# Optimization experiments

Measured on AMD Instinct MI355X. Metric: run time of the kernel, lower is better.

## Reference

```python
import jax, jax.numpy as jnp
import numpy as np

N = 50000
E = 600000
IN_CH = 128
HID = 64


def setup_inputs() -> dict:
    key = jax.random.key(0)
    ks = jax.random.split(key, 8)
    x = jax.random.normal(ks[0], (N, IN_CH), dtype=jnp.float32)
    edge_index = jax.random.randint(ks[1], (2, E), 0, N, dtype=jnp.int64)
    s = 1.0 / np.sqrt(IN_CH)
    W_rel = jax.random.uniform(ks[2], (IN_CH, HID), jnp.float32, -s, s)
    b_rel = jax.random.uniform(ks[3], (HID,), jnp.float32, -s, s)
    W_root = jax.random.uniform(ks[4], (IN_CH, HID), jnp.float32, -s, s)
    sh = 1.0 / np.sqrt(HID)
    W_dec = jax.random.uniform(ks[5], (HID, IN_CH), jnp.float32, -sh, sh)
    b_dec = jax.random.uniform(ks[6], (IN_CH,), jnp.float32, -sh, sh)
    return {"x": x, "edge_index": edge_index, "W_rel": W_rel, "b_rel": b_rel,
            "W_root": W_root, "W_dec": W_dec, "b_dec": b_dec}


def reference(x, edge_index, W_rel, b_rel, W_root, W_dec, b_dec):
    src, dst = edge_index[0], edge_index[1]
    # gather source node features, sum-aggregate at destination nodes  [N, IN_CH]
    agg = jax.ops.segment_sum(x[src], dst, num_segments=N)
    # GraphConv: lin_rel(agg) + lin_root(x)  (lin_rel carries the bias)
    h = agg @ W_rel + b_rel + x @ W_root
    h = jax.nn.relu(h)
    # linear decoder back to input feature space
    return h @ W_dec + b_dec
```

## Files before the change

### kernel.cpp

```cpp
#include <hip/hip_runtime.h>

#define IN_CH 128
#define HID 64
#define ELLW 32
#define SPILLCAP 4096
#define LSPCAP 128
#define NSCAT 256
#define BCAP 3584

typedef short v8s __attribute__((ext_vector_type(8)));
typedef float v4f __attribute__((ext_vector_type(4)));

__device__ __forceinline__ unsigned int bf16pair(float a, float b) {
    unsigned int ua = __float_as_uint(a);
    unsigned int ub = __float_as_uint(b);
    ua = (ua + 0x7fffu + ((ua >> 16) & 1u)) >> 16;
    ub = (ub + 0x7fffu + ((ub >> 16) & 1u)) & 0xffff0000u;
    return ua | ub;
}
__device__ __forceinline__ unsigned short bf16of(float a) {
    unsigned int ua = __float_as_uint(a);
    return (unsigned short)((ua + 0x7fffu + ((ua >> 16) & 1u)) >> 16);
}

__global__ __launch_bounds__(256) void graphmae_prep(
    const float* __restrict__ W_rel, const float* __restrict__ W_root,
    const float* __restrict__ W_dec,
    unsigned short* __restrict__ Bt, unsigned short* __restrict__ Wdt,
    int* __restrict__ bucketcur, int NZ)
{
    const int idx = blockIdx.x * 256 + threadIdx.x;
    if (idx < NZ) bucketcur[idx] = 0;
    if (idx < 16384) {
        const int k = idx >> 7;
        const int c = idx & 127;
        const float v = (c < HID) ? W_rel[(size_t)k * HID + c]
                                  : W_root[(size_t)k * HID + (c - HID)];
        Bt[(size_t)c * 128 + k] = bf16of(v);
    } else if (idx < 24576) {
        const int j = idx - 16384;
        const int k = j >> 7;
        const int c = j & 127;
        Wdt[(size_t)c * 64 + k] = bf16of(W_dec[(size_t)k * IN_CH + c]);
    }
}

__global__ __launch_bounds__(512) void graphmae_encode_scatter(
    const float* __restrict__ x, const unsigned short* __restrict__ Bt,
    const float* __restrict__ b_rel, const int* __restrict__ ei,
    unsigned short* __restrict__ y16, unsigned short* __restrict__ agg16,
    int* __restrict__ bucketcur, unsigned int* __restrict__ sorted,
    int* __restrict__ spillcnt, int2* __restrict__ spill,
    int N, int E, int NBUK, int CE)
{
    __shared__ int lh[256];
    __shared__ int lcur[256];

    const int t  = threadIdx.x;
    const int n0 = blockIdx.x * 64;
    const bool sduty = (blockIdx.x < NSCAT);
    const int e0 = blockIdx.x * CE;
    const int e1 = sduty ? min(E, e0 + CE) : 0;

    if (t >= 256) { lh[t - 256] = 0; lcur[t - 256] = 0; }
    __syncthreads();

    if (t < 256) {
        const int w    = t >> 6;
        const int lane = t & 63;
        const int mr   = lane & 15;
        const int kg   = lane >> 4;
        const int nrow = n0 + w * 16 + mr;

        v8s xfrag[4];
        #pragma unroll
        for (int ks = 0; ks < 4; ++ks) {
            uint4 pk = make_uint4(0u, 0u, 0u, 0u);
            if (nrow < N) {
                const float* xp = x + (size_t)nrow * IN_CH + ks * 32 + kg * 8;
                const float4 u0 = *(const float4*)(xp);
                const float4 u1 = *(const float4*)(xp + 4);
                pk = make_uint4(bf16pair(u0.x, u0.y), bf16pair(u0.z, u0.w),
                                bf16pair(u1.x, u1.y), bf16pair(u1.z, u1.w));
            }
            xfrag[ks] = *(v8s*)&pk;
        }

        #pragma unroll
        for (int ct = 0; ct < 8; ++ct) {
            v4f acc = {0.f, 0.f, 0.f, 0.f};
            const unsigned short* bp = Bt + (size_t)(ct * 16 + mr) * 128 + kg * 8;
            #pragma unroll
            for (int ks = 0; ks < 4; ++ks) {
                const v8s b = *(const v8s*)(bp + ks * 32);
                acc = __builtin_amdgcn_mfma_f32_16x16x32_bf16(b, xfrag[ks], acc, 0, 0, 0);
            }
            if (nrow < N) {
                if (ct < 4) {
                    const int c = ct * 16 + kg * 4;
                    *(uint2*)(y16 + (size_t)nrow * HID + c) =
                        make_uint2(bf16pair(acc[0], acc[1]), bf16pair(acc[2], acc[3]));
                } else {
                    const int c = (ct - 4) * 16 + kg * 4;
                    const float4 br = *(const float4*)(b_rel + c);
                    *(uint2*)(agg16 + (size_t)nrow * HID + c) =
                        make_uint2(bf16pair(acc[0] + br.x, acc[1] + br.y),
                                   bf16pair(acc[2] + br.z, acc[3] + br.w));
                }
            }
        }
    } else if (sduty) {
        for (int e = e0 + (t - 256); e < e1; e += 256)
            atomicAdd(&lh[ei[E + e] >> 8], 1);
    }
    __syncthreads();

    if (t >= 256 && sduty) {
        const int b = t - 256;
        if (b < NBUK) {
            const int cnt = lh[b];
            if (cnt > 0) lcur[b] = atomicAdd(&bucketcur[b], cnt);
        }
    }
    __syncthreads();

    if (t >= 256 && sduty) {
        for (int e = e0 + (t - 256); e < e1; e += 256) {
            const int d = ei[E + e];
            const int s = ei[e];
            const int b = d >> 8;
            const int pos = atomicAdd(&lcur[b], 1);
            if (pos < BCAP) {
                sorted[(size_t)b * BCAP + pos] =
                    ((unsigned)(d & 255) << 16) | (unsigned)s;
            } else {
                const int p = atomicAdd(spillcnt, 1);
                if (p < SPILLCAP) spill[p] = make_int2(d, s);
            }
        }
    }
}

__global__ __launch_bounds__(256) void bucket_gather_decode(
    const unsigned int* __restrict__ sorted, const int* __restrict__ bucketcur,
    const unsigned short* __restrict__ y16, const unsigned short* __restrict__ agg16,
    const int* __restrict__ spillcnt, const int2* __restrict__ spill,
    const unsigned short* __restrict__ Wdt, const float* __restrict__ b_dec,
    float* __restrict__ out, int N)
{
    __shared__ unsigned short sl[32 * ELLW];
    __shared__ int cnt[32];
    __shared__ int lsp[LSPCAP];
    __shared__ int lspcnt;
    __shared__ unsigned short hs[32][72];

    const int t   = threadIdx.x;
    const int b   = blockIdx.x >> 3;
    const int spl = blockIdx.x & 7;
    const int dlo = spl * 32;

    if (t < 32) cnt[t] = 0;
    if (t == 32) lspcnt = 0;
    __syncthreads();

    const int m = min(bucketcur[b], BCAP);
    const unsigned int* src = sorted + (size_t)b * BCAP;
    for (int i = t; i < m; i += 256) {
        const unsigned int v = src[i];
        const int dl = (int)(v >> 16) - dlo;
        if ((unsigned)dl < 32u) {
            const int r = atomicAdd(&cnt[dl], 1);
            if (r < ELLW) {
                sl[dl * ELLW + r] = (unsigned short)(v & 0xffffu);
            } else {
                const int p = atomicAdd(&lspcnt, 1);
                if (p < LSPCAP) lsp[p] = (dl << 16) | (int)(v & 0xffffu);
            }
        }
    }
    __syncthreads();

    const int wid  = t >> 6;
    const int lane = t & 63;
    const int es   = lane >> 3;
    const int cl   = lane & 7;
    const int lspN = min(lspcnt, LSPCAP);
    const int spN  = min(*spillcnt, SPILLCAP);

    for (int j = 0; j < 8; ++j) {
        const int dl = wid * 8 + j;
        const int n  = (b << 8) + dlo + dl;
        if (n >= N) continue;
        const int c_ = min(cnt[dl], ELLW);
        const unsigned short* sp = sl + dl * ELLW;

        uint4 av = make_uint4(0u, 0u, 0u, 0u);
        if (es == 0) av = *(const uint4*)(agg16 + (size_t)n * HID + cl * 8);

        float acc[8];
        #pragma unroll
        for (int q = 0; q < 8; ++q) acc[q] = 0.f;

        for (int e = es; e < c_; e += 8) {
            const int s = sp[e];
            const uint4 v = *(const uint4*)(y16 + (size_t)s * HID + cl * 8);
            acc[0] += __uint_as_float(v.x << 16);
            acc[1] += __uint_as_float(v.x & 0xffff0000u);
            acc[2] += __uint_as_float(v.y << 16);
            acc[3] += __uint_as_float(v.y & 0xffff0000u);
            acc[4] += __uint_as_float(v.z << 16);
            acc[5] += __uint_as_float(v.z & 0xffff0000u);
            acc[6] += __uint_as_float(v.w << 16);
            acc[7] += __uint_as_float(v.w & 0xffff0000u);
        }
        for (int i = es; i < lspN; i += 8) {
            const int e2 = lsp[i];
            if ((e2 >> 16) == dl) {
                const int s = e2 & 0xffff;
                const uint4 v = *(const uint4*)(y16 + (size_t)s * HID + cl * 8);
                acc[0] += __uint_as_float(v.x << 16);
                acc[1] += __uint_as_float(v.x & 0xffff0000u);
                acc[2] += __uint_as_float(v.y << 16);
                acc[3] += __uint_as_float(v.y & 0xffff0000u);
                acc[4] += __uint_as_float(v.z << 16);
                acc[5] += __uint_as_float(v.z & 0xffff0000u);
                acc[6] += __uint_as_float(v.w << 16);
                acc[7] += __uint_as_float(v.w & 0xffff0000u);
            }
        }
        for (int i = es; i < spN; i += 8) {
            const int2 e2 = spill[i];
            if (e2.x == n) {
                const uint4 v = *(const uint4*)(y16 + (size_t)e2.y * HID + cl * 8);
                acc[0] += __uint_as_float(v.x << 16);
                acc[1] += __uint_as_float(v.x & 0xffff0000u);
                acc[2] += __uint_as_float(v.y << 16);
                acc[3] += __uint_as_float(v.y & 0xffff0000u);
                acc[4] += __uint_as_float(v.z << 16);
                acc[5] += __uint_as_float(v.z & 0xffff0000u);
                acc[6] += __uint_as_float(v.w << 16);
                acc[7] += __uint_as_float(v.w & 0xffff0000u);
            }
        }

        #pragma unroll
        for (int mk = 8; mk <= 32; mk <<= 1) {
            #pragma unroll
            for (int q = 0; q < 8; ++q) acc[q] += __shfl_xor(acc[q], mk);
        }

        if (es == 0) {
            const float h0 = fmaxf(__uint_as_float(av.x << 16)          + acc[0], 0.f);
            const float h1 = fmaxf(__uint_as_float(av.x & 0xffff0000u) + acc[1], 0.f);
            const float h2 = fmaxf(__uint_as_float(av.y << 16)          + acc[2], 0.f);
            const float h3 = fmaxf(__uint_as_float(av.y & 0xffff0000u) + acc[3], 0.f);
            const float h4 = fmaxf(__uint_as_float(av.z << 16)          + acc[4], 0.f);
            const float h5 = fmaxf(__uint_as_float(av.z & 0xffff0000u) + acc[5], 0.f);
            const float h6 = fmaxf(__uint_as_float(av.w << 16)          + acc[6], 0.f);
            const float h7 = fmaxf(__uint_as_float(av.w & 0xffff0000u) + acc[7], 0.f);
            uint4 o;
            o.x = bf16pair(h0, h1);
            o.y = bf16pair(h2, h3);
            o.z = bf16pair(h4, h5);
            o.w = bf16pair(h6, h7);
            *(uint4*)(&hs[dl][cl * 8]) = o;
        }
    }
    __syncthreads();

    const int mr   = lane & 15;
    const int kg   = lane >> 4;
    const int tile = wid & 1;
    const int ct0  = (wid >> 1) * 4;
    const int nrow = (b << 8) + dlo + tile * 16 + mr;

    v8s hfrag[2];
    #pragma unroll
    for (int ks = 0; ks < 2; ++ks)
        hfrag[ks] = *(const v8s*)(&hs[tile * 16 + mr][ks * 32 + kg * 8]);

    #pragma unroll
    for (int ct = ct0; ct < ct0 + 4; ++ct) {
        v4f acc = {0.f, 0.f, 0.f, 0.f};
        const unsigned short* wp = Wdt + (size_t)(ct * 16 + mr) * 64 + kg * 8;
        #pragma unroll
        for (int ks = 0; ks < 2; ++ks) {
            const v8s bb = *(const v8s*)(wp + ks * 32);
            acc = __builtin_amdgcn_mfma_f32_16x16x32_bf16(bb, hfrag[ks], acc, 0, 0, 0);
        }
        if (nrow < N) {
            const int c = ct * 16 + kg * 4;
            const float4 bd = *(const float4*)(b_dec + c);
            *(float4*)(out + (size_t)nrow * IN_CH + c) =
                make_float4(acc[0] + bd.x, acc[1] + bd.y,
                            acc[2] + bd.z, acc[3] + bd.w);
        }
    }
}

extern "C" void kernel_launch(void* const* d_in, const int* in_sizes, int n_in,
                              void* d_out, int out_size, void* d_ws, size_t ws_size,
                              hipStream_t stream)
{
    const float* x      = (const float*)d_in[0];
    const int*   ei     = (const int*)  d_in[1];
    const float* W_rel  = (const float*)d_in[2];
    const float* b_rel  = (const float*)d_in[3];
    const float* W_root = (const float*)d_in[4];
    const float* W_dec  = (const float*)d_in[5];
    const float* b_dec  = (const float*)d_in[6];
    float* out = (float*)d_out;

    const int N = in_sizes[0] / IN_CH;
    const int E = in_sizes[1] / 2;

    const int NBUK = (N + 255) / 256;
    const int CE   = (E + NSCAT - 1) / NSCAT;

    unsigned short* y16   = (unsigned short*)d_ws;
    unsigned short* agg16 = y16 + (size_t)N * HID;
    unsigned int* sorted  = (unsigned int*)(agg16 + (size_t)N * HID);
    int* bucketcur = (int*)(sorted + (size_t)NBUK * BCAP);
    int* spillcnt  = bucketcur + NBUK;
    int2* spill    = (int2*)(spillcnt + 3);
    unsigned short* Bt  = (unsigned short*)(spill + SPILLCAP);
    unsigned short* Wdt = Bt + 128 * 128;

    const int nblk64 = (N + 63) / 64;

    graphmae_prep<<<96, 256, 0, stream>>>(W_rel, W_root, W_dec, Bt, Wdt,
                                          bucketcur, NBUK + 1);

    graphmae_encode_scatter<<<nblk64, 512, 0, stream>>>(
        x, Bt, b_rel, ei, y16, agg16,
        bucketcur, sorted, spillcnt, spill, N, E, NBUK, CE);

    bucket_gather_decode<<<NBUK * 8, 256, 0, stream>>>(
        sorted, bucketcur, y16, agg16, spillcnt, spill, Wdt, b_dec, out, N);
}
```

Measured before the change: 70.96 us.

## Fuse prep, encode/scatter and gather/decode into one cooperative persistent kernel

```diff
diff --git a/kernel.cpp b/kernel.cpp
--- a/kernel.cpp
+++ b/kernel.cpp
@@ -1,4 +1,7 @@
 #include <hip/hip_runtime.h>
+#include <hip/hip_cooperative_groups.h>
+
+namespace cg = cooperative_groups;
 
 #define IN_CH 128
 #define HID 64
@@ -23,6 +26,269 @@
     return (unsigned short)((ua + 0x7fffu + ((ua >> 16) & 1u)) >> 16);
 }
 
+__global__ __launch_bounds__(256, 6) void graphmae_fused(
+    const float* __restrict__ x, const int* __restrict__ ei,
+    const float* __restrict__ W_rel, const float* __restrict__ b_rel,
+    const float* __restrict__ W_root, const float* __restrict__ W_dec,
+    const float* __restrict__ b_dec, float* __restrict__ out,
+    unsigned short* __restrict__ y16, unsigned short* __restrict__ agg16,
+    unsigned int* __restrict__ sorted, int* __restrict__ bucketcur,
+    int* __restrict__ spillcnt, int2* __restrict__ spill,
+    unsigned short* __restrict__ Bt, unsigned short* __restrict__ Wdt,
+    int N, int E, int NBUK, int CE)
+{
+    cg::grid_group grid = cg::this_grid();
+
+    __shared__ int lh[256];
+    __shared__ int lcur[256];
+    __shared__ unsigned short sl[32 * ELLW];
+    __shared__ int cnt[32];
+    __shared__ int lsp[LSPCAP];
+    __shared__ int lspcnt;
+    __shared__ unsigned short hs[32][72];
+
+    const int t  = threadIdx.x;
+    const int GD = gridDim.x;
+
+    for (int idx = blockIdx.x * 256 + t; idx < 24576; idx += GD * 256) {
+        if (idx < 16384) {
+            const int k = idx >> 7, c = idx & 127;
+            const float v = (c < HID) ? W_rel[(size_t)k * HID + c]
+                                      : W_root[(size_t)k * HID + (c - HID)];
+            Bt[(size_t)c * 128 + k] = bf16of(v);
+        } else {
+            const int j = idx - 16384;
+            const int k = j >> 7, c = j & 127;
+            Wdt[(size_t)c * 64 + k] = bf16of(W_dec[(size_t)k * IN_CH + c]);
+        }
+    }
+    for (int idx = blockIdx.x * 256 + t; idx < NBUK + 1; idx += GD * 256) {
+        if (idx < NBUK) bucketcur[idx] = 0;
+        else *spillcnt = 0;
+    }
+    grid.sync();
+
+    const int NUNITE = NSCAT + ((N + 63) >> 6);
+    for (int u = blockIdx.x; u < NUNITE; u += GD) {
+        if (u < NSCAT) {
+            lh[t] = 0; lcur[t] = 0;
+            __syncthreads();
+            const int e0 = u * CE, e1 = min(E, e0 + CE);
+            for (int e = e0 + t; e < e1; e += 256)
+                atomicAdd(&lh[ei[E + e] >> 8], 1);
+            __syncthreads();
+            if (t < NBUK) {
+                const int c0 = lh[t];
+                if (c0 > 0) lcur[t] = atomicAdd(&bucketcur[t], c0);
+            }
+            __syncthreads();
+            for (int e = e0 + t; e < e1; e += 256) {
+                const int d = ei[E + e];
+                const int s = ei[e];
+                const int bb = d >> 8;
+                const int pos = atomicAdd(&lcur[bb], 1);
+                if (pos < BCAP) {
+                    sorted[(size_t)bb * BCAP + pos] =
+                        ((unsigned)(d & 255) << 16) | (unsigned)s;
+                } else {
+                    const int p = atomicAdd(spillcnt, 1);
+                    if (p < SPILLCAP) spill[p] = make_int2(d, s);
+                }
+            }
+        } else {
+            const int n0   = (u - NSCAT) * 64;
+            const int w    = t >> 6;
+            const int lane = t & 63;
+            const int mr   = lane & 15;
+            const int kg   = lane >> 4;
+            const int nrow = n0 + w * 16 + mr;
+
+            v8s xfrag[4];
+            #pragma unroll
+            for (int ks = 0; ks < 4; ++ks) {
+                uint4 pk = make_uint4(0u, 0u, 0u, 0u);
+                if (nrow < N) {
+                    const float* xp = x + (size_t)nrow * IN_CH + ks * 32 + kg * 8;
+                    const float4 u0 = *(const float4*)(xp);
+                    const float4 u1 = *(const float4*)(xp + 4);
+                    pk = make_uint4(bf16pair(u0.x, u0.y), bf16pair(u0.z, u0.w),
+                                    bf16pair(u1.x, u1.y), bf16pair(u1.z, u1.w));
+                }
+                xfrag[ks] = *(v8s*)&pk;
+            }
+
+            #pragma unroll
+            for (int ct = 0; ct < 8; ++ct) {
+                v4f acc = {0.f, 0.f, 0.f, 0.f};
+                const unsigned short* bp = Bt + (size_t)(ct * 16 + mr) * 128 + kg * 8;
+                #pragma unroll
+                for (int ks = 0; ks < 4; ++ks) {
+                    const v8s bb = *(const v8s*)(bp + ks * 32);
+                    acc = __builtin_amdgcn_mfma_f32_16x16x32_bf16(bb, xfrag[ks], acc, 0, 0, 0);
+                }
+                if (nrow < N) {
+                    if (ct < 4) {
+                        const int c = ct * 16 + kg * 4;
+                        *(uint2*)(y16 + (size_t)nrow * HID + c) =
+                            make_uint2(bf16pair(acc[0], acc[1]), bf16pair(acc[2], acc[3]));
+                    } else {
+                        const int c = (ct - 4) * 16 + kg * 4;
+                        const float4 br = *(const float4*)(b_rel + c);
+                        *(uint2*)(agg16 + (size_t)nrow * HID + c) =
+                            make_uint2(bf16pair(acc[0] + br.x, acc[1] + br.y),
+                                       bf16pair(acc[2] + br.z, acc[3] + br.w));
+                    }
+                }
+            }
+        }
+    }
+    grid.sync();
+
+    const int NUNITG = NBUK * 8;
+    for (int v = blockIdx.x; v < NUNITG; v += GD) {
+        const int b   = v >> 3;
+        const int spl = v & 7;
+        const int dlo = spl * 32;
+
+        if (t < 32) cnt[t] = 0;
+        if (t == 32) lspcnt = 0;
+        __syncthreads();
+
+        const int m = min(bucketcur[b], BCAP);
+        const unsigned int* src = sorted + (size_t)b * BCAP;
+        for (int i = t; i < m; i += 256) {
+            const unsigned int vv = src[i];
+            const int dl = (int)(vv >> 16) - dlo;
+            if ((unsigned)dl < 32u) {
+                const int r = atomicAdd(&cnt[dl], 1);
+                if (r < ELLW) sl[dl * ELLW + r] = (unsigned short)(vv & 0xffffu);
+                else {
+                    const int p = atomicAdd(&lspcnt, 1);
+                    if (p < LSPCAP) lsp[p] = (dl << 16) | (int)(vv & 0xffffu);
+                }
+            }
+        }
+        __syncthreads();
+
+        const int wid  = t >> 6;
+        const int lane = t & 63;
+        const int es   = lane >> 3;
+        const int cl   = lane & 7;
+        const int lspN = min(lspcnt, LSPCAP);
+        const int spN  = min(*spillcnt, SPILLCAP);
+
+        for (int j = 0; j < 8; ++j) {
+            const int dl = wid * 8 + j;
+            const int n  = (b << 8) + dlo + dl;
+            if (n >= N) continue;
+            const int c_ = min(cnt[dl], ELLW);
+            const unsigned short* sp = sl + dl * ELLW;
+
+            uint4 av = make_uint4(0u, 0u, 0u, 0u);
+            if (es == 0) av = *(const uint4*)(agg16 + (size_t)n * HID + cl * 8);
+
+            float acc[8];
+            #pragma unroll
+            for (int q = 0; q < 8; ++q) acc[q] = 0.f;
+
+            for (int e = es; e < c_; e += 8) {
+                const int s = sp[e];
+                const uint4 vv = *(const uint4*)(y16 + (size_t)s * HID + cl * 8);
+                acc[0] += __uint_as_float(vv.x << 16);
+                acc[1] += __uint_as_float(vv.x & 0xffff0000u);
+                acc[2] += __uint_as_float(vv.y << 16);
+                acc[3] += __uint_as_float(vv.y & 0xffff0000u);
+                acc[4] += __uint_as_float(vv.z << 16);
+                acc[5] += __uint_as_float(vv.z & 0xffff0000u);
+                acc[6] += __uint_as_float(vv.w << 16);
+                acc[7] += __uint_as_float(vv.w & 0xffff0000u);
+            }
+            for (int i = es; i < lspN; i += 8) {
+                const int e2 = lsp[i];
+                if ((e2 >> 16) == dl) {
+                    const int s = e2 & 0xffff;
+                    const uint4 vv = *(const uint4*)(y16 + (size_t)s * HID + cl * 8);
+                    acc[0] += __uint_as_float(vv.x << 16);
+                    acc[1] += __uint_as_float(vv.x & 0xffff0000u);
+                    acc[2] += __uint_as_float(vv.y << 16);
+                    acc[3] += __uint_as_float(vv.y & 0xffff0000u);
+                    acc[4] += __uint_as_float(vv.z << 16);
+                    acc[5] += __uint_as_float(vv.z & 0xffff0000u);
+                    acc[6] += __uint_as_float(vv.w << 16);
+                    acc[7] += __uint_as_float(vv.w & 0xffff0000u);
+                }
+            }
+            for (int i = es; i < spN; i += 8) {
+                const int2 e2 = spill[i];
+                if (e2.x == n) {
+                    const uint4 vv = *(const uint4*)(y16 + (size_t)e2.y * HID + cl * 8);
+                    acc[0] += __uint_as_float(vv.x << 16);
+                    acc[1] += __uint_as_float(vv.x & 0xffff0000u);
+                    acc[2] += __uint_as_float(vv.y << 16);
+                    acc[3] += __uint_as_float(vv.y & 0xffff0000u);
+                    acc[4] += __uint_as_float(vv.z << 16);
+                    acc[5] += __uint_as_float(vv.z & 0xffff0000u);
+                    acc[6] += __uint_as_float(vv.w << 16);
+                    acc[7] += __uint_as_float(vv.w & 0xffff0000u);
+                }
+            }
+
+            #pragma unroll
+            for (int mk = 8; mk <= 32; mk <<= 1) {
+                #pragma unroll
+                for (int q = 0; q < 8; ++q) acc[q] += __shfl_xor(acc[q], mk);
+            }
+
+            if (es == 0) {
+                const float h0 = fmaxf(__uint_as_float(av.x << 16)          + acc[0], 0.f);
+                const float h1 = fmaxf(__uint_as_float(av.x & 0xffff0000u) + acc[1], 0.f);
+                const float h2 = fmaxf(__uint_as_float(av.y << 16)          + acc[2], 0.f);
+                const float h3 = fmaxf(__uint_as_float(av.y & 0xffff0000u) + acc[3], 0.f);
+                const float h4 = fmaxf(__uint_as_float(av.z << 16)          + acc[4], 0.f);
+                const float h5 = fmaxf(__uint_as_float(av.z & 0xffff0000u) + acc[5], 0.f);
+                const float h6 = fmaxf(__uint_as_float(av.w << 16)          + acc[6], 0.f);
+                const float h7 = fmaxf(__uint_as_float(av.w & 0xffff0000u) + acc[7], 0.f);
+                uint4 o;
+                o.x = bf16pair(h0, h1);
+                o.y = bf16pair(h2, h3);
+                o.z = bf16pair(h4, h5);
+                o.w = bf16pair(h6, h7);
+                *(uint4*)(&hs[dl][cl * 8]) = o;
+            }
+        }
+        __syncthreads();
+
+        const int mr   = lane & 15;
+        const int kg   = lane >> 4;
+        const int tile = wid & 1;
+        const int ct0  = (wid >> 1) * 4;
+        const int nrow = (b << 8) + dlo + tile * 16 + mr;
+
+        v8s hfrag[2];
+        #pragma unroll
+        for (int ks = 0; ks < 2; ++ks)
+            hfrag[ks] = *(const v8s*)(&hs[tile * 16 + mr][ks * 32 + kg * 8]);
+
+        #pragma unroll
+        for (int ct = ct0; ct < ct0 + 4; ++ct) {
+            v4f acc = {0.f, 0.f, 0.f, 0.f};
+            const unsigned short* wp = Wdt + (size_t)(ct * 16 + mr) * 64 + kg * 8;
+            #pragma unroll
+            for (int ks = 0; ks < 2; ++ks) {
+                const v8s bb = *(const v8s*)(wp + ks * 32);
+                acc = __builtin_amdgcn_mfma_f32_16x16x32_bf16(bb, hfrag[ks], acc, 0, 0, 0);
+            }
+            if (nrow < N) {
+                const int c = ct * 16 + kg * 4;
+                const float4 bd = *(const float4*)(b_dec + c);
+                *(float4*)(out + (size_t)nrow * IN_CH + c) =
+                    make_float4(acc[0] + bd.x, acc[1] + bd.y,
+                                acc[2] + bd.z, acc[3] + bd.w);
+            }
+        }
+    }
+}
+
 __global__ __launch_bounds__(256) void graphmae_prep(
     const float* __restrict__ W_rel, const float* __restrict__ W_root,
     const float* __restrict__ W_dec,
@@ -32,15 +298,13 @@
     const int idx = blockIdx.x * 256 + threadIdx.x;
     if (idx < NZ) bucketcur[idx] = 0;
     if (idx < 16384) {
-        const int k = idx >> 7;
-        const int c = idx & 127;
+        const int k = idx >> 7, c = idx & 127;
         const float v = (c < HID) ? W_rel[(size_t)k * HID + c]
                                   : W_root[(size_t)k * HID + (c - HID)];
         Bt[(size_t)c * 128 + k] = bf16of(v);
     } else if (idx < 24576) {
         const int j = idx - 16384;
-        const int k = j >> 7;
-        const int c = j & 127;
+        const int k = j >> 7, c = j & 127;
         Wdt[(size_t)c * 64 + k] = bf16of(W_dec[(size_t)k * IN_CH + c]);
     }
 }
@@ -92,8 +356,8 @@
             const unsigned short* bp = Bt + (size_t)(ct * 16 + mr) * 128 + kg * 8;
             #pragma unroll
             for (int ks = 0; ks < 4; ++ks) {
-                const v8s b = *(const v8s*)(bp + ks * 32);
-                acc = __builtin_amdgcn_mfma_f32_16x16x32_bf16(b, xfrag[ks], acc, 0, 0, 0);
+                const v8s bb = *(const v8s*)(bp + ks * 32);
+                acc = __builtin_amdgcn_mfma_f32_16x16x32_bf16(bb, xfrag[ks], acc, 0, 0, 0);
             }
             if (nrow < N) {
                 if (ct < 4) {
@@ -118,8 +382,8 @@
     if (t >= 256 && sduty) {
         const int b = t - 256;
         if (b < NBUK) {
-            const int cnt = lh[b];
-            if (cnt > 0) lcur[b] = atomicAdd(&bucketcur[b], cnt);
+            const int c0 = lh[b];
+            if (c0 > 0) lcur[b] = atomicAdd(&bucketcur[b], c0);
         }
     }
     __syncthreads();
@@ -170,9 +434,8 @@
         const int dl = (int)(v >> 16) - dlo;
         if ((unsigned)dl < 32u) {
             const int r = atomicAdd(&cnt[dl], 1);
-            if (r < ELLW) {
-                sl[dl * ELLW + r] = (unsigned short)(v & 0xffffu);
-            } else {
+            if (r < ELLW) sl[dl * ELLW + r] = (unsigned short)(v & 0xffffu);
+            else {
                 const int p = atomicAdd(&lspcnt, 1);
                 if (p < LSPCAP) lsp[p] = (dl << 16) | (int)(v & 0xffffu);
             }
@@ -326,15 +589,33 @@
     unsigned short* Bt  = (unsigned short*)(spill + SPILLCAP);
     unsigned short* Wdt = Bt + 128 * 128;
 
-    const int nblk64 = (N + 63) / 64;
-
-    graphmae_prep<<<96, 256, 0, stream>>>(W_rel, W_root, W_dec, Bt, Wdt,
-                                          bucketcur, NBUK + 1);
-
-    graphmae_encode_scatter<<<nblk64, 512, 0, stream>>>(
-        x, Bt, b_rel, ei, y16, agg16,
-        bucketcur, sorted, spillcnt, spill, N, E, NBUK, CE);
-
-    bucket_gather_decode<<<NBUK * 8, 256, 0, stream>>>(
-        sorted, bucketcur, y16, agg16, spillcnt, spill, Wdt, b_dec, out, N);
+    int mb = 0;
+    hipError_t qe = hipOccupancyMaxActiveBlocksPerMultiprocessor(
+        &mb, graphmae_fused, 256, 0);
+    int g = (qe == hipSuccess && mb > 0) ? mb * 256 : 0;
+    if (g > NBUK * 8) g = NBUK * 8;
+
+    hipError_t le = hipErrorUnknown;
+    if (g >= 256) {
+        int Ni = N, Ei = E, NBUKi = NBUK, CEi = CE;
+        void* args[] = {
+            (void*)&x, (void*)&ei, (void*)&W_rel, (void*)&b_rel,
+            (void*)&W_root, (void*)&W_dec, (void*)&b_dec, (void*)&out,
+            (void*)&y16, (void*)&agg16, (void*)&sorted, (void*)&bucketcur,
+            (void*)&spillcnt, (void*)&spill, (void*)&Bt, (void*)&Wdt,
+            (void*)&Ni, (void*)&Ei, (void*)&NBUKi, (void*)&CEi };
+        le = hipLaunchCooperativeKernel((void*)graphmae_fused,
+                                        dim3(g), dim3(256), args, 0, stream);
+    }
+
+    if (le != hipSuccess) {
+        const int nblk64 = (N + 63) / 64;
+        graphmae_prep<<<96, 256, 0, stream>>>(W_rel, W_root, W_dec, Bt, Wdt,
+                                              bucketcur, NBUK + 1);
+        graphmae_encode_scatter<<<nblk64, 512, 0, stream>>>(
+            x, Bt, b_rel, ei, y16, agg16,
+            bucketcur, sorted, spillcnt, spill, N, E, NBUK, CE);
+        bucket_gather_decode<<<NBUK * 8, 256, 0, stream>>>(
+            sorted, bucketcur, y16, agg16, spillcnt, spill, Wdt, b_dec, out, N);
+    }
 }
```

Result: slower. 248.5 us (+250.2%).
